# Performance work log

Hardware: AMD Instinct MI355X
Metric: run time of the kernel (lower is better)

## Reference

```python
import jax, jax.numpy as jnp
import numpy as np

IMG = 512
SIZES = (16, 32, 64, 128, 256)
FEAT_HW = (128, 64, 32, 16, 8)
STRIDES = tuple(IMG // h for h in FEAT_HW)
RATIOS = np.array([0.5, 1.0, 2.0])
PRE_NMS = 1000        # pre_nms_top_n['testing']
POST_NMS = 300        # post_nms_top_n['testing']
NMS_THRESH = 0.7
MIN_SIZE = 1e-3
BBOX_XFORM_CLIP = float(np.log(1000.0 / 16.0))


def _base_anchors(size):
    h_r = np.sqrt(RATIOS)
    w_r = 1.0 / h_r
    ws = w_r * size
    hs = h_r * size
    return np.round(np.stack([-ws, -hs, ws, hs], axis=1) / 2.0)  # [3,4]


def _level_anchors(size, stride, hw):
    ba = _base_anchors(size)
    s = np.arange(hw, dtype=np.float32) * stride
    yy, xx = np.meshgrid(s, s, indexing='ij')  # y-major like torchvision
    shifts = np.stack([xx.ravel(), yy.ravel(), xx.ravel(), yy.ravel()], axis=1)
    return (shifts[:, None, :] + ba[None, :, :]).reshape(-1, 4).astype(np.float32)


ANCHORS = [jnp.asarray(_level_anchors(SIZES[i], STRIDES[i], FEAT_HW[i])) for i in range(5)]


def _conv(x, w, b, pad):
    y = jax.lax.conv_general_dilated(x, w, (1, 1), [(pad, pad), (pad, pad)],
                                     dimension_numbers=('NCHW', 'OIHW', 'NCHW'))
    return y + b[None, :, None, None]


def _decode(deltas, anchors):
    # deltas [N,K,4], anchors [K,4]; BoxCoder weights (1,1,1,1)
    w = anchors[:, 2] - anchors[:, 0]
    h = anchors[:, 3] - anchors[:, 1]
    cx = anchors[:, 0] + 0.5 * w
    cy = anchors[:, 1] + 0.5 * h
    dx, dy = deltas[..., 0], deltas[..., 1]
    dw = jnp.minimum(deltas[..., 2], BBOX_XFORM_CLIP)
    dh = jnp.minimum(deltas[..., 3], BBOX_XFORM_CLIP)
    pcx = dx * w + cx
    pcy = dy * h + cy
    pw = jnp.exp(dw) * w
    ph = jnp.exp(dh) * h
    return jnp.stack([pcx - 0.5 * pw, pcy - 0.5 * ph,
                      pcx + 0.5 * pw, pcy + 0.5 * ph], axis=-1)


def _nms_single(boxes_off, scores_masked, boxes_raw, scores_raw):
    # greedy NMS over fixed POST_NMS steps; suppressed/invalid score = -1
    def step(s, _):
        i = jnp.argmax(s)
        ok = s[i] > -0.5
        b = boxes_off[i]
        lt = jnp.maximum(b[:2], boxes_off[:, :2])
        rb = jnp.minimum(b[2:], boxes_off[:, 2:])
        wh = jnp.clip(rb - lt, 0.0)
        inter = wh[:, 0] * wh[:, 1]
        area_i = (b[2] - b[0]) * (b[3] - b[1])
        areas = (boxes_off[:, 2] - boxes_off[:, 0]) * (boxes_off[:, 3] - boxes_off[:, 1])
        iou = inter / jnp.maximum(area_i + areas - inter, 1e-9)
        s = jnp.where(ok & (iou > NMS_THRESH), -1.0, s)
        s = s.at[i].set(-1.0)
        return s, (i, ok)

    _, (idx, ok) = jax.lax.scan(step, scores_masked, None, length=POST_NMS)
    out_b = jnp.where(ok[:, None], boxes_raw[idx], 0.0)
    out_s = jnp.where(ok, scores_raw[idx], 0.0)
    return out_b, out_s


def _rpn_forward(feats, conv_w, conv_b, cls_w, cls_b, bbox_w, bbox_b):
    all_s, all_b, lvl_ids = [], [], []
    for lvl, f in enumerate(feats):
        t = jax.nn.relu(_conv(f, conv_w, conv_b, 1))
        obj = _conv(t, cls_w, cls_b, 0)      # [N,3,H,W]
        reg = _conv(t, bbox_w, bbox_b, 0)    # [N,12,H,W]
        N, _, H, W = obj.shape
        obj = obj.transpose(0, 2, 3, 1).reshape(N, -1)  # (H,W,A) order
        reg = reg.reshape(N, 3, 4, H, W).transpose(0, 3, 4, 1, 2).reshape(N, -1, 4)
        boxes = _decode(reg, ANCHORS[lvl])              # [N,HWA,4]
        k = min(PRE_NMS, obj.shape[1])
        top_s, top_i = jax.lax.top_k(obj, k)
        boxes = jnp.take_along_axis(boxes, top_i[:, :, None], axis=1)
        all_s.append(top_s)
        all_b.append(boxes)
        lvl_ids.append(jnp.full((k,), float(lvl), dtype=jnp.float32))
    scores = jnp.concatenate(all_s, axis=1)   # [N,K]
    boxes = jnp.concatenate(all_b, axis=1)    # [N,K,4]
    lvl = jnp.concatenate(lvl_ids)            # [K]
    # clip to image (512x512)
    boxes = jnp.stack([jnp.clip(boxes[..., 0], 0.0, IMG), jnp.clip(boxes[..., 1], 0.0, IMG),
                       jnp.clip(boxes[..., 2], 0.0, IMG), jnp.clip(boxes[..., 3], 0.0, IMG)], axis=-1)
    valid = ((boxes[..., 2] - boxes[..., 0]) >= MIN_SIZE) & ((boxes[..., 3] - boxes[..., 1]) >= MIN_SIZE)
    prob = jax.nn.sigmoid(scores)
    masked = jnp.where(valid, prob, -1.0)
    # batched_nms trick: offset boxes per level so cross-level IoU is 0
    off = lvl * (IMG + 1.0)
    boxes_off = boxes + off[None, :, None]
    return jax.vmap(_nms_single)(boxes_off, masked, boxes, prob)


def setup_inputs() -> dict:
    key = jax.random.key(0)
    ks = jax.random.split(key, 12)
    N, C = 4, 256
    inp = {'images': jax.random.normal(ks[0], (N, 3, IMG, IMG), jnp.float32)}
    for i, hw in enumerate(FEAT_HW):
        inp[f'f{i}'] = jax.random.normal(ks[1 + i], (N, C, hw, hw), jnp.float32)
    inp['conv_w'] = jax.random.normal(ks[6], (C, C, 3, 3), jnp.float32) * 0.01
    inp['conv_b'] = jnp.zeros((C,), jnp.float32)
    inp['cls_w'] = jax.random.normal(ks[7], (3, C, 1, 1), jnp.float32) * 0.01
    inp['cls_b'] = jnp.zeros((3,), jnp.float32)
    inp['bbox_w'] = jax.random.normal(ks[8], (12, C, 1, 1), jnp.float32) * 0.01
    inp['bbox_b'] = jnp.zeros((12,), jnp.float32)
    return inp


def reference(images, f0, f1, f2, f3, f4, conv_w, conv_b, cls_w, cls_b, bbox_w, bbox_b):
    # images only determine the (static) image size used for clipping
    del images
    return _rpn_forward((f0, f1, f2, f3, f4), conv_w, conv_b, cls_w, cls_b, bbox_w, bbox_b)
```

## Files before the change

kernel.cpp:

```cpp
#include <hip/hip_runtime.h>

#define FULL_PER_IMG 65472
#define SEL_PER_IMG  3960
#define BBOX_CLIP    4.135166556742356f

__device__ __forceinline__ unsigned int sortkey(float f){
  unsigned int u = __float_as_uint(f);
  return (u & 0x80000000u) ? ~u : (u | 0x80000000u);
}

__global__ __launch_bounds__(256) void repack_w(const float* __restrict__ src,
                                                float* __restrict__ dst){
  int idx = blockIdx.x*256 + threadIdx.x;
  if (idx >= 786432) return;
  int t  = idx % 12;
  int rc = idx / 12;
  int co = rc & 255;
  int ci = rc >> 8;
  dst[idx] = (t < 9) ? src[co*2304 + ci*9 + t] : 0.f;
}

#define CHBUF 1536
#define SMEMF 4160

template<int TX, int H, int NBX>
__device__ void conv_level(int lb,
    const float* __restrict__ f, int strd, float asize, int full_off, float lvl,
    const float* __restrict__ wp, const float* __restrict__ conv_b,
    const float* __restrict__ cls_w, const float* __restrict__ cls_b,
    const float* __restrict__ bbox_w, const float* __restrict__ bbox_b,
    float* __restrict__ A_score, float* __restrict__ A_masked, float* __restrict__ A_boxoff,
    float* smem, float (*s_out)[16])
{
  constexpr int W    = H;
  constexpr int NBY  = H/2;
  constexpr int P    = 2*TX;
  constexpr int ROWW = TX + 4;
  constexpr int CIST = 4*ROWW;
  constexpr int CHFL = 32*CIST;
  constexpr int NSTG = (CHFL + 255)/256;

  const int xb = lb % NBX;
  const int yb = (lb / NBX) % NBY;
  const int n  = lb / (NBX*NBY);
  const int x0 = xb * TX;
  const int y0 = yb * 2;
  const int co = threadIdx.x;
  const float* Fn = f + (size_t)n*256*H*W;
  float* lds_stage = smem;
  float* lds_t     = smem;

  float acc[2][TX];
  #pragma unroll
  for (int o=0;o<2;o++)
    #pragma unroll
    for (int p=0;p<TX;p++) acc[o][p] = conv_b[co];

  int soff[NSTG];
  #pragma unroll
  for (int k=0;k<NSTG;k++){
    const int e  = co + k*256;
    const int cl = e / CIST;
    const int rem = e - cl*CIST;
    const int r  = rem / ROWW;
    const int j  = rem - r*ROWW;
    const int yg = y0 - 1 + r, xg = x0 - 1 + j;
    soff[k] = (e < CHFL && yg>=0 && yg<H && xg>=0 && xg<W)
            ? (cl*H + yg)*W + xg : -1;
  }

#define STAGE(CB, BUF) do {                                                  \
    const float* Fb_ = Fn + (size_t)(CB)*H*W;                                \
    float st_[NSTG];                                                         \
    _Pragma("unroll")                                                        \
    for (int k=0;k<NSTG;k++)                                                 \
      st_[k] = (soff[k] >= 0) ? Fb_[soff[k]] : 0.f;                          \
    _Pragma("unroll")                                                        \
    for (int k=0;k<NSTG;k++){                                                \
      const int e = co + k*256;                                              \
      if (e < CHFL) (BUF)[e] = st_[k];                                       \
    }                                                                        \
  } while(0)

#define CIFMA(SB, CL, WV) do {                                               \
    const float* bp_ = (SB) + (CL)*CIST;                                     \
    _Pragma("unroll")                                                        \
    for (int r=0;r<4;r++){                                                   \
      float rw_[ROWW];                                                       \
      _Pragma("unroll")                                                      \
      for (int q=0;q<ROWW/4;q++){                                            \
        float4 v_ = *(const float4*)(bp_ + r*ROWW + 4*q);                    \
        rw_[4*q+0]=v_.x; rw_[4*q+1]=v_.y;                                    \
        rw_[4*q+2]=v_.z; rw_[4*q+3]=v_.w;                                    \
      }                                                                      \
      if (r <= 2){                                                           \
        _Pragma("unroll")                                                    \
        for (int kx=0;kx<3;kx++){                                            \
          const float w_ = WV[r*3+kx];                                       \
          _Pragma("unroll")                                                  \
          for (int p=0;p<TX;p++) acc[0][p] = fmaf(w_, rw_[p+kx], acc[0][p]); \
        }                                                                    \
      }                                                                      \
      if (r >= 1){                                                           \
        _Pragma("unroll")                                                    \
        for (int kx=0;kx<3;kx++){                                            \
          const float w_ = WV[(r-1)*3+kx];                                   \
          _Pragma("unroll")                                                  \
          for (int p=0;p<TX;p++) acc[1][p] = fmaf(w_, rw_[p+kx], acc[1][p]); \
        }                                                                    \
      }                                                                      \
    }                                                                        \
  } while(0)

  STAGE(0, lds_stage);
  __syncthreads();

  for (int ch=0; ch<8; ++ch){
    const float* sb = lds_stage + (ch&1)*CHBUF;
    for (int cl=0; cl<32; ++cl){
      const int ci = ch*32 + cl;
      const float* wrow = wp + ((size_t)ci*256 + (size_t)co)*12;
      float4 wA = *(const float4*)(wrow);
      float4 wB = *(const float4*)(wrow + 4);
      float  w8 = wrow[8];
      float wv[9] = {wA.x,wA.y,wA.z,wA.w, wB.x,wB.y,wB.z,wB.w, w8};
      CIFMA(sb, cl, wv);
    }
    if (ch<7){
      STAGE((ch+1)*32, lds_stage + ((ch+1)&1)*CHBUF);
      __syncthreads();
    }
  }
#undef STAGE
#undef CIFMA

  __syncthreads();

  #pragma unroll
  for (int o=0;o<2;o++)
    #pragma unroll
    for (int p=0;p<TX;p++) lds_t[(o*TX+p)*260+co] = fmaxf(acc[o][p], 0.f);
  __syncthreads();

  {
    const int p = threadIdx.x % P;
    const int o = threadIdx.x / P;
    if (o < 15){
      const float* w1 = (o<3) ? (cls_w + o*256) : (bbox_w + (o-3)*256);
      float s = (o<3) ? cls_b[o] : bbox_b[o-3];
      const float4* wl = (const float4*)w1;
      const float4* tl = (const float4*)(lds_t + p*260);
      #pragma unroll 8
      for (int c=0;c<64;c++){
        float4 a = wl[c], b = tl[c];
        s += a.x*b.x + a.y*b.y + a.z*b.z + a.w*b.w;
      }
      s_out[o][p] = s;
    }
  }
  __syncthreads();

  if (threadIdx.x < 3*P){
    const int p = threadIdx.x / 3;
    const int a = threadIdx.x % 3;
    const int px = p % TX;
    const int yo = y0 + p / TX;
    float sraw = s_out[a][p];
    float dx = s_out[3+a*4+0][p];
    float dy = s_out[3+a*4+1][p];
    float dw = fminf(s_out[3+a*4+2][p], BBOX_CLIP);
    float dh = fminf(s_out[3+a*4+3][p], BBOX_CLIP);
    float ratio = (a==0)?0.5f:((a==1)?1.0f:2.0f);
    float hr = sqrtf(ratio);
    float wh2 = rintf(asize / hr * 0.5f);
    float hh2 = rintf(asize * hr * 0.5f);
    float w = 2.f*wh2, h = 2.f*hh2;
    float cx = (float)((x0+px)*strd);
    float cy = (float)(yo*strd);
    float pcx = dx*w + cx, pcy = dy*h + cy;
    float pw = expf(dw)*w, ph = expf(dh)*h;
    float x1 = pcx - 0.5f*pw, y1 = pcy - 0.5f*ph;
    float x2 = pcx + 0.5f*pw, y2 = pcy + 0.5f*ph;
    x1 = fminf(fmaxf(x1,0.f),512.f); y1 = fminf(fmaxf(y1,0.f),512.f);
    x2 = fminf(fmaxf(x2,0.f),512.f); y2 = fminf(fmaxf(y2,0.f),512.f);
    bool valid = ((x2-x1) >= 1e-3f) && ((y2-y1) >= 1e-3f);
    float prob = 1.f/(1.f+expf(-sraw));
    float masked = valid ? prob : -1.f;
    float off = lvl*513.f;
    size_t gi = (size_t)n*FULL_PER_IMG + full_off + ((yo*W + (x0+px))*3 + a);
    A_score[gi]  = sraw;
    A_masked[gi] = masked;
    float4 bo; bo.x=x1+off; bo.y=y1+off; bo.z=x2+off; bo.w=y2+off;
    *(float4*)(A_boxoff + gi*4) = bo;
  }
}

__global__ __launch_bounds__(256)
void conv_all(
    const float* __restrict__ f0, const float* __restrict__ f1,
    const float* __restrict__ f2, const float* __restrict__ f3,
    const float* __restrict__ f4,
    const float* __restrict__ wp, const float* __restrict__ conv_b,
    const float* __restrict__ cls_w, const float* __restrict__ cls_b,
    const float* __restrict__ bbox_w, const float* __restrict__ bbox_b,
    float* __restrict__ A_score, float* __restrict__ A_masked, float* __restrict__ A_boxoff)
{
  __shared__ float smem[SMEMF];
  __shared__ float s_out[15][16];
  const int b = blockIdx.x;
  if (b < 4096)
    conv_level< 8,128,16>(b,      f0,  4,  16.f,     0, 0.f, wp, conv_b, cls_w, cls_b, bbox_w, bbox_b, A_score, A_masked, A_boxoff, smem, s_out);
  else if (b < 5120)
    conv_level< 8, 64, 8>(b-4096, f1,  8,  32.f, 49152, 1.f, wp, conv_b, cls_w, cls_b, bbox_w, bbox_b, A_score, A_masked, A_boxoff, smem, s_out);
  else if (b < 5376)
    conv_level< 8, 32, 4>(b-5120, f2, 16,  64.f, 61440, 2.f, wp, conv_b, cls_w, cls_b, bbox_w, bbox_b, A_score, A_masked, A_boxoff, smem, s_out);
  else if (b < 5504)
    conv_level< 4, 16, 4>(b-5376, f3, 32, 128.f, 64512, 3.f, wp, conv_b, cls_w, cls_b, bbox_w, bbox_b, A_score, A_masked, A_boxoff, smem, s_out);
  else
    conv_level< 4,  8, 2>(b-5504, f4, 64, 256.f, 65280, 4.f, wp, conv_b, cls_w, cls_b, bbox_w, bbox_b, A_score, A_masked, A_boxoff, smem, s_out);
}

__global__ __launch_bounds__(1024) void select_kernel(
    const float* __restrict__ A_score, const float* __restrict__ A_masked,
    const float* __restrict__ A_boxoff,
    float* __restrict__ C_masked, float* __restrict__ C_boxoff)
{
  const int b = blockIdx.x;
  const int tid = threadIdx.x;
  if (b >= 12){
    const int n = b - 12;
    if (tid < 960){
      size_t gF = (size_t)n*FULL_PER_IMG + 64512 + tid;
      size_t gS = (size_t)n*SEL_PER_IMG  + 3000 + tid;
      C_masked[gS] = A_masked[gF];
      *(float4*)(C_boxoff + gS*4) = *(const float4*)(A_boxoff + gF*4);
    }
    return;
  }
  const int n = b / 3, lvl = b % 3;
  const int HWAs[3]  = {49152, 12288, 3072};
  const int FOFF[3]  = {0, 49152, 61440};
  const int HWA = HWAs[lvl];
  const size_t baseF = (size_t)n*FULL_PER_IMG + FOFF[lvl];
  const size_t baseS = (size_t)n*SEL_PER_IMG + lvl*1000;
  const int k = 1000;
  const int wid = tid >> 6;

  __shared__ unsigned int hist[16][256];
  __shared__ unsigned int histM[256];
  __shared__ unsigned int sh_prefix, sh_krem, sh_c0, sh_c1, sh_above;
  if (tid==0){ sh_prefix=0u; sh_krem=(unsigned)k; }
  __syncthreads();

  for (int pass=3; pass>=0; pass--){
    unsigned int* hp = &hist[0][0];
    for (int z=tid; z<4096; z+=1024) hp[z] = 0u;
    __syncthreads();
    unsigned int pfx = sh_prefix;
    for (int i=tid;i<HWA;i+=1024){
      unsigned int u = sortkey(A_score[baseF+i]);
      if (pass==3 || (u >> ((pass+1)*8)) == pfx)
        atomicAdd(&hist[wid][(u>>(pass*8)) & 255u], 1u);
    }
    __syncthreads();
    if (tid < 256){
      unsigned int s = 0u;
      #pragma unroll
      for (int w=0;w<16;w++) s += hist[w][tid];
      histM[tid] = s;
    }
    __syncthreads();
    if (tid==0){
      unsigned int krem = sh_krem, accum = 0u; int chosen = 0;
      for (int bb=255; bb>=0; bb--){
        if (accum + histM[bb] >= krem){ chosen = bb; break; }
        accum += histM[bb];
      }
      sh_krem   = krem - accum;
      sh_prefix = (pfx<<8) | (unsigned)chosen;
    }
    __syncthreads();
  }
  const unsigned int T = sh_prefix;
  if (tid==0){ sh_c0=0u; sh_c1=0u; sh_above = (unsigned)k - sh_krem; }
  __syncthreads();
  const unsigned int nAbove = sh_above, need = sh_krem;

  for (int i=tid;i<HWA;i+=1024){
    unsigned int u = sortkey(A_score[baseF+i]);
    int pos = -1;
    if (u > T) pos = (int)atomicAdd(&sh_c0,1u);
    else if (u == T){
      unsigned int t = atomicAdd(&sh_c1,1u);
      if (t < need) pos = (int)(nAbove + t);
    }
    if (pos >= 0){
      C_masked[baseS+pos] = A_masked[baseF+i];
      *(float4*)(C_boxoff + (baseS+pos)*4) = *(const float4*)(A_boxoff + (baseF+i)*4);
    }
  }
}

__global__ __launch_bounds__(256) void nms_kernel(
    const float* __restrict__ C_masked, const float* __restrict__ C_boxoff,
    float* __restrict__ out_b, float* __restrict__ out_s)
{
  const int n = blockIdx.x, tid = threadIdx.x;
  __shared__ unsigned long long keys[4096];
  __shared__ float4 bcache[1024];
  __shared__ float accb[304][4];

  #pragma unroll
  for (int s=0; s<16; ++s){
    int i = s*256 + tid;
    unsigned long long kk = 0ull;
    if (i < SEL_PER_IMG){
      unsigned int sk = sortkey(C_masked[(size_t)n*SEL_PER_IMG + i]);
      kk = ((unsigned long long)sk << 32) | (unsigned int)(~(unsigned int)i);
    }
    keys[i] = kk;
  }
  __syncthreads();

  for (int k = 2; k <= 4096; k <<= 1){
    for (int j = k >> 1; j > 0; j >>= 1){
      #pragma unroll
      for (int s=0; s<16; ++s){
        int i = s*256 + tid;
        int ixj = i ^ j;
        if (ixj > i){
          unsigned long long a = keys[i], b = keys[ixj];
          bool up = ((i & k) == 0);
          bool sw = up ? (a < b) : (a > b);
          if (sw){ keys[i] = b; keys[ixj] = a; }
        }
      }
      __syncthreads();
    }
  }

  for (int s=tid; s<1024; s+=256){
    int idx = (int)(~(unsigned int)keys[s]);
    bcache[s] = *(const float4*)(C_boxoff + ((size_t)n*SEL_PER_IMG + idx)*4);
  }
  __syncthreads();

  if (tid >= 64) return;
  const unsigned int THRK = sortkey(-0.5f);
  int nAcc = 0;
  unsigned long long kk = keys[0];
  float4 bx = bcache[0];
  for (int i = 0; i < 4096 && nAcc < 300; ++i){
    unsigned long long kn = (i+1 < 4096) ? keys[i+1] : 0ull;
    unsigned int khin = (unsigned int)(kn >> 32);
    float4 bnext = make_float4(0.f,0.f,0.f,0.f);
    if (i+1 < 1024) bnext = bcache[i+1];
    else if (khin > THRK){
      int idn = (int)(~(unsigned int)kn);
      bnext = *(const float4*)(C_boxoff + ((size_t)n*SEL_PER_IMG + idn)*4);
    }
    unsigned int khi = (unsigned int)(kk >> 32);
    if (khi <= THRK) break;
    bool sup = false;
    #pragma unroll
    for (int q=0; q<5; ++q){
      int a = tid + q*64;
      if (a < nAcc){
        float a0=accb[a][0], a1=accb[a][1], a2=accb[a][2], a3=accb[a][3];
        float xx1 = fmaxf(a0, bx.x), yy1 = fmaxf(a1, bx.y);
        float xx2 = fminf(a2, bx.z), yy2 = fminf(a3, bx.w);
        float iw = fmaxf(xx2-xx1, 0.f), ih = fmaxf(yy2-yy1, 0.f);
        float inter = iw*ih;
        float ar_a = (a2-a0)*(a3-a1);
        float ar_b = (bx.z-bx.x)*(bx.w-bx.y);
        float iou = inter / fmaxf(ar_a + ar_b - inter, 1e-9f);
        sup |= (iou > 0.7f);
      }
    }
    if (__ballot(sup) == 0ull){
      if (tid == 0){
        accb[nAcc][0]=bx.x; accb[nAcc][1]=bx.y; accb[nAcc][2]=bx.z; accb[nAcc][3]=bx.w;
        int idx = (int)(~(unsigned int)kk);
        int lvl = (idx<1000)?0:((idx<2000)?1:((idx<3000)?2:((idx<3768)?3:4)));
        float off = (float)lvl * 513.f;
        size_t ob = ((size_t)n*300 + nAcc)*4;
        out_b[ob+0]=bx.x-off; out_b[ob+1]=bx.y-off; out_b[ob+2]=bx.z-off; out_b[ob+3]=bx.w-off;
        out_s[(size_t)n*300 + nAcc] = __uint_as_float(khi & 0x7fffffffu);
      }
      ++nAcc;
    }
    kk = kn; bx = bnext;
  }
}

extern "C" void kernel_launch(void* const* d_in, const int* in_sizes, int n_in,
                              void* d_out, int out_size, void* d_ws, size_t ws_size,
                              hipStream_t stream) {
  (void)in_sizes; (void)n_in; (void)ws_size;
  const float* f0     = (const float*)d_in[1];
  const float* f1     = (const float*)d_in[2];
  const float* f2     = (const float*)d_in[3];
  const float* f3     = (const float*)d_in[4];
  const float* f4     = (const float*)d_in[5];
  const float* conv_w = (const float*)d_in[6];
  const float* conv_b = (const float*)d_in[7];
  const float* cls_w  = (const float*)d_in[8];
  const float* cls_b  = (const float*)d_in[9];
  const float* bbox_w = (const float*)d_in[10];
  const float* bbox_b = (const float*)d_in[11];

  float* ws       = (float*)d_ws;
  float* wp       = ws;
  float* A_score  = wp       + 786432;
  float* A_masked = A_score  + 261888;
  float* A_boxoff = A_masked + 261888;
  float* C_masked = A_boxoff + 1047552;
  float* C_boxoff = C_masked + 15840;

  float* out_b = (float*)d_out;
  float* out_s = out_b + 4800;

  hipMemsetAsync(d_out, 0, (size_t)out_size*sizeof(float), stream);

  repack_w<<<3072, 256, 0, stream>>>(conv_w, wp);

  conv_all<<<5536, 256, 0, stream>>>(f0, f1, f2, f3, f4,
      wp, conv_b, cls_w, cls_b, bbox_w, bbox_b, A_score, A_masked, A_boxoff);

  select_kernel<<<16, 1024, 0, stream>>>(A_score, A_masked, A_boxoff, C_masked, C_boxoff);
  nms_kernel<<<4, 256, 0, stream>>>(C_masked, C_boxoff, out_b, out_s);
}
```

Before: 1.867 ms.

## Repack conv weights tap-major for coalesced loads and drop row register copies

Conv weights are repacked as [ci][tap][co], so each thread reads its 9 weights with stride 256 across taps. Adjacent threads (co) therefore read adjacent floats, which coalesces the global weight loads; before, each thread issued per-thread float4 loads from a 48-byte stride. The LDS row reads now keep three float4 values and index them with compile-time macros instead of copying into a local array, which may reduce register pressure. In exchange there are 9 scalar loads per input channel instead of 2 vector loads plus 1 scalar.

```diff
diff --git a/kernel.cpp b/kernel.cpp
--- a/kernel.cpp
+++ b/kernel.cpp
@@ -12,12 +12,11 @@
 __global__ __launch_bounds__(256) void repack_w(const float* __restrict__ src,
                                                 float* __restrict__ dst){
   int idx = blockIdx.x*256 + threadIdx.x;
-  if (idx >= 786432) return;
-  int t  = idx % 12;
-  int rc = idx / 12;
-  int co = rc & 255;
-  int ci = rc >> 8;
-  dst[idx] = (t < 9) ? src[co*2304 + ci*9 + t] : 0.f;
+  if (idx >= 589824) return;
+  int co = idx & 255;
+  int kt = idx >> 8;
+  int ci = kt / 9, tap = kt % 9;
+  dst[idx] = src[co*2304 + ci*9 + tap];
 }
 
 #define CHBUF 1536
@@ -82,23 +81,23 @@
     }                                                                        \
   } while(0)
 
+#define CMP4_(Q,I) ((I)==0?(Q).x:((I)==1?(Q).y:((I)==2?(Q).z:(Q).w)))
+#define EL_(I) ((I)<4 ? CMP4_(q0_,(I)) : ((I)<8 ? CMP4_(q1_,(I)-4) : CMP4_(q2_,(I)-8)))
+
 #define CIFMA(SB, CL, WV) do {                                               \
     const float* bp_ = (SB) + (CL)*CIST;                                     \
     _Pragma("unroll")                                                        \
     for (int r=0;r<4;r++){                                                   \
-      float rw_[ROWW];                                                       \
-      _Pragma("unroll")                                                      \
-      for (int q=0;q<ROWW/4;q++){                                            \
-        float4 v_ = *(const float4*)(bp_ + r*ROWW + 4*q);                    \
-        rw_[4*q+0]=v_.x; rw_[4*q+1]=v_.y;                                    \
-        rw_[4*q+2]=v_.z; rw_[4*q+3]=v_.w;                                    \
-      }                                                                      \
+      float4 q0_ = *(const float4*)(bp_ + r*ROWW);                           \
+      float4 q1_ = *(const float4*)(bp_ + r*ROWW + 4);                       \
+      float4 q2_ = (ROWW > 8) ? *(const float4*)(bp_ + r*ROWW + 8)           \
+                              : make_float4(0.f,0.f,0.f,0.f);                \
       if (r <= 2){                                                           \
         _Pragma("unroll")                                                    \
         for (int kx=0;kx<3;kx++){                                            \
           const float w_ = WV[r*3+kx];                                       \
           _Pragma("unroll")                                                  \
-          for (int p=0;p<TX;p++) acc[0][p] = fmaf(w_, rw_[p+kx], acc[0][p]); \
+          for (int p=0;p<TX;p++) acc[0][p] = fmaf(w_, EL_(p+kx), acc[0][p]); \
         }                                                                    \
       }                                                                      \
       if (r >= 1){                                                           \
@@ -106,7 +105,7 @@
         for (int kx=0;kx<3;kx++){                                            \
           const float w_ = WV[(r-1)*3+kx];                                   \
           _Pragma("unroll")                                                  \
-          for (int p=0;p<TX;p++) acc[1][p] = fmaf(w_, rw_[p+kx], acc[1][p]); \
+          for (int p=0;p<TX;p++) acc[1][p] = fmaf(w_, EL_(p+kx), acc[1][p]); \
         }                                                                    \
       }                                                                      \
     }                                                                        \
@@ -119,11 +118,10 @@
     const float* sb = lds_stage + (ch&1)*CHBUF;
     for (int cl=0; cl<32; ++cl){
       const int ci = ch*32 + cl;
-      const float* wrow = wp + ((size_t)ci*256 + (size_t)co)*12;
-      float4 wA = *(const float4*)(wrow);
-      float4 wB = *(const float4*)(wrow + 4);
-      float  w8 = wrow[8];
-      float wv[9] = {wA.x,wA.y,wA.z,wA.w, wB.x,wB.y,wB.z,wB.w, w8};
+      float wv[9];
+      const float* wrow = wp + (size_t)ci*2304 + co;
+      #pragma unroll
+      for (int t=0;t<9;t++) wv[t] = wrow[t*256];
       CIFMA(sb, cl, wv);
     }
     if (ch<7){
@@ -133,6 +131,8 @@
   }
 #undef STAGE
 #undef CIFMA
+#undef EL_
+#undef CMP4_
 
   __syncthreads();
 
@@ -411,7 +411,7 @@
 
   float* ws       = (float*)d_ws;
   float* wp       = ws;
-  float* A_score  = wp       + 786432;
+  float* A_score  = wp       + 589824;
   float* A_masked = A_score  + 261888;
   float* A_boxoff = A_masked + 261888;
   float* C_masked = A_boxoff + 1047552;
@@ -422,7 +422,7 @@
 
   hipMemsetAsync(d_out, 0, (size_t)out_size*sizeof(float), stream);
 
-  repack_w<<<3072, 256, 0, stream>>>(conv_w, wp);
+  repack_w<<<2304, 256, 0, stream>>>(conv_w, wp);
 
   conv_all<<<5536, 256, 0, stream>>>(f0, f1, f2, f3, f4,
       wp, conv_b, cls_w, cls_b, bbox_w, bbox_b, A_score, A_masked, A_boxoff);
```

Result: faster. 1.826 ms (-2.2%).
